# Kernel optimization log

Hardware: AMD Instinct MI355X
Metric: run time of the kernel (lower is better)

Reference implementation:

```python
import jax, jax.numpy as jnp
import numpy as np


def _dct_basis(n: int) -> jnp.ndarray:
    # Unnormalized DCT-II basis matching torch_dct.dct(norm=None):
    # X[k] = 2 * sum_n x[n] * cos(pi*(2n+1)*k / (2N))
    k = np.arange(n)[:, None]
    m = np.arange(n)[None, :]
    D = 2.0 * np.cos(np.pi * (2.0 * m + 1.0) * k / (2.0 * n))
    return jnp.asarray(D, dtype=jnp.float32)


def setup_inputs() -> dict:
    key = jax.random.key(0)
    img = jax.random.normal(key, (32, 3, 512, 512), dtype=jnp.float32)
    return {"img": img}


def reference(img) -> jnp.ndarray:
    B, C, H, W = img.shape
    Dh = _dct_basis(H)  # [H, H]
    Dw = _dct_basis(W)  # [W, W]
    x = img.astype(jnp.float32)
    # 2D DCT-II: Dh @ x @ Dw^T, batched over (B, C); fused /1000 scale.
    tmp = jnp.einsum('kh,bchw->bckw', Dh, x)
    out = jnp.einsum('bckw,lw->bckl', tmp, Dw) / 1000.0
    return out
```

## Files before the change

kernel.cpp:

```cpp
#include <hip/hip_runtime.h>
#include <hip/hip_bf16.h>
#include <stdint.h>

#define NPIX 512
#define NBC  96
#define NWG8 (NBC * 4)
#define NWG13 (NBC * 8)

typedef __attribute__((ext_vector_type(8))) short bf16x8;
typedef __attribute__((ext_vector_type(4))) float f32x4;
typedef __attribute__((ext_vector_type(8))) unsigned short u16x8;

__device__ __forceinline__ unsigned short f2bf(float f) {
    __hip_bfloat16 h = __float2bfloat16(f);
    union { __hip_bfloat16 h; unsigned short u; } v;
    v.h = h;
    return v.u;
}

#define GLD16(g, l) __builtin_amdgcn_global_load_lds( \
    (const __attribute__((address_space(1))) void*)(const void*)(g), \
    (__attribute__((address_space(3))) void*)(void*)(l), 16, 0, 0)

#define SBAR() do { __builtin_amdgcn_sched_barrier(0); \
                    __builtin_amdgcn_s_barrier(); \
                    __builtin_amdgcn_sched_barrier(0); } while (0)
#define LGKM0() do { asm volatile("s_waitcnt lgkmcnt(0)" ::: "memory"); \
                     __builtin_amdgcn_sched_barrier(0); } while (0)
#define SB0() __builtin_amdgcn_sched_barrier(0)
#define VMW(n) do { asm volatile("s_waitcnt vmcnt(" #n ")" ::: "memory"); } while (0)

__global__ void k_basis(unsigned short* __restrict__ D) {
    int idx = blockIdx.x * 256 + threadIdx.x;
    int k = idx >> 9, n = idx & 511;
    int m = ((2 * n + 1) * k) & 2047;
    float ang = (float)m * 3.06796157577128218e-03f;
    D[idx] = f2bf(2.0f * cosf(ang));
}

__global__ __launch_bounds__(512, 4) void k_s1x(
        const unsigned short* __restrict__ D,
        const float* __restrict__ X,
        unsigned short* __restrict__ sT) {
    __shared__ __align__(16) char LDS[81920];

    const int bid = blockIdx.x;
    const int nb  = (bid & 7) * (NWG13 / 8) + (bid >> 3);
    const int bc = nb >> 3, mt = (nb >> 2) & 1, nt = nb & 3;
    const int mA0 = mt * 256, nB0 = nt * 128;
    const unsigned short* Aimg = D;
    const float* Bimg = X + (size_t)bc * NPIX * NPIX;

    const int tid  = threadIdx.x;
    const int lane = tid & 63;
    const int wid  = tid >> 6;
    const int wr = wid >> 2, wc = wid & 3;
    const int rm = lane & 15;
    const int kq = lane >> 4;

    f32x4 acc[8][2] = {};
    bf16x8 a[4], b[2];

    auto stageA = [&](int kt, int p2, int H) {
        int c = tid;
        int rp = c >> 2, g = c & 3;
        int gs = g ^ ((rp >> 1) & 3);
        int row = ((rp >> 6) << 7) + H * 64 + (rp & 63);
        GLD16(Aimg + (size_t)(mA0 + row) * NPIX + kt * 32 + gs * 8,
              LDS + p2 * 16384 + H * 8192 + c * 16);
    };
    auto stageB = [&](int kt, int s3, int H) {
        int c = tid;
        int rp = c >> 3, g = c & 7;
        int gs = g ^ (rp & 7);
        int row = ((rp >> 5) << 6) + H * 32 + (rp & 31);
        GLD16(Bimg + (size_t)(nB0 + row) * NPIX + kt * 32 + gs * 4,
              LDS + 32768 + s3 * 16384 + H * 8192 + c * 16);
    };
    auto readA = [&](int p2, int mh) {
        const char* base = LDS + p2 * 16384 + mh * 8192;
        #pragma unroll
        for (int f = 0; f < 4; ++f) {
            int rp = wr * 64 + f * 16 + rm;
            int slot = kq ^ ((rm >> 1) & 3);
            a[f] = *(const bf16x8*)(base + rp * 64 + slot * 16);
        }
    };
    auto readB = [&](int s3) {
        const char* base = LDS + 32768 + s3 * 16384 + (wc & 1) * 8192;
        #pragma unroll
        for (int jj = 0; jj < 2; ++jj) {
            int rp = (wc >> 1) * 32 + jj * 16 + rm;
            const char* rb = base + rp * 128;
            f32x4 v0 = *(const f32x4*)(rb + (((kq * 2 + 0) ^ (rm & 7)) * 16));
            f32x4 v1 = *(const f32x4*)(rb + (((kq * 2 + 1) ^ (rm & 7)) * 16));
            bf16x8 t;
            t[0] = (short)f2bf(v0[0]); t[1] = (short)f2bf(v0[1]);
            t[2] = (short)f2bf(v0[2]); t[3] = (short)f2bf(v0[3]);
            t[4] = (short)f2bf(v1[0]); t[5] = (short)f2bf(v1[1]);
            t[6] = (short)f2bf(v1[2]); t[7] = (short)f2bf(v1[3]);
            b[jj] = t;
        }
    };
    auto mma = [&](int mh) {
        __builtin_amdgcn_s_setprio(1);
        #pragma unroll
        for (int f = 0; f < 4; ++f)
            #pragma unroll
            for (int jj = 0; jj < 2; ++jj)
                acc[mh * 4 + f][jj] = __builtin_amdgcn_mfma_f32_16x16x32_bf16(
                    a[f], b[jj], acc[mh * 4 + f][jj], 0, 0, 0);
        __builtin_amdgcn_s_setprio(0);
    };

    stageB(0, 0, 0); SB0();
    stageB(0, 0, 1); SB0();
    stageA(0, 0, 0); SB0();
    stageA(0, 0, 1); SB0();
    stageB(1, 1, 0); SB0();
    stageB(1, 1, 1); SB0();

    for (int T = 0; T < 14; ++T) {
        const int p2 = T & 1, p2n = p2 ^ 1;
        const int s3 = T % 3, s3b = (T + 2) % 3;
        VMW(3); SBAR();
        readA(p2, 0); readB(s3);
        stageA(T + 1, p2n, 0); SB0();
        stageB(T + 2, s3b, 0); SB0();
        LGKM0(); mma(0);
        VMW(3); SBAR();
        readA(p2, 1);
        stageA(T + 1, p2n, 1); SB0();
        stageB(T + 2, s3b, 1); SB0();
        LGKM0(); mma(1);
    }
    {
        VMW(3); SBAR();
        readA(0, 0); readB(2);
        stageA(15, 1, 0); SB0();
        LGKM0(); mma(0);
        VMW(2); SBAR();
        readA(0, 1);
        stageA(15, 1, 1); SB0();
        LGKM0(); mma(1);
    }
    {
        VMW(1); SBAR();
        readA(1, 0); readB(0);
        LGKM0(); mma(0);
        VMW(0); SBAR();
        readA(1, 1);
        LGKM0(); mma(1);
    }

    unsigned short* Co = sT + (size_t)bc * NPIX * NPIX;
    #pragma unroll
    for (int mh = 0; mh < 2; ++mh)
        #pragma unroll
        for (int f = 0; f < 4; ++f) {
            int l_ = mA0 + wr * 128 + mh * 64 + f * 16 + kq * 4;
            #pragma unroll
            for (int jj = 0; jj < 2; ++jj) {
                int h_ = nB0 + wc * 32 + jj * 16 + rm;
                f32x4 v = acc[mh * 4 + f][jj];
                #pragma unroll
                for (int r = 0; r < 4; ++r)
                    Co[(size_t)(l_ + r) * NPIX + h_] = f2bf(v[r]);
            }
        }
}

__global__ __launch_bounds__(512) void k_s2g(
        const unsigned short* __restrict__ D,
        const unsigned short* __restrict__ sT,
        float* __restrict__ Cv) {
    __shared__ __align__(16) char LDS[131072];

    const int bid = blockIdx.x;
    const int nb  = (bid & 7) * (NWG8 / 8) + (bid >> 3);
    const int bc = nb >> 2, mt = (nb >> 1) & 1, nt = nb & 1;
    const int mA0 = mt * 256, nB0 = nt * 256;
    const unsigned short* Aimg = D;
    const unsigned short* Bimg = sT + (size_t)bc * NPIX * NPIX;

    const int tid  = threadIdx.x;
    const int lane = tid & 63;
    const int wid  = tid >> 6;
    const int wr = wid >> 2, wc = wid & 3;
    const int rm = lane & 15;
    const int kq = lane >> 4;

    f32x4 acc[8][4] = {};
    bf16x8 a[4][2], b0[2][2], b1[2][2];

    auto stageA = [&](int kt, int p, int H) {
        char* dst = LDS + p * 32768 + H * 16384;
        #pragma unroll
        for (int it = 0; it < 2; ++it) {
            int c = it * 512 + tid;
            int rp = c >> 3, g = c & 7;
            int gs = g ^ (rp & 7);
            int row = ((rp >> 6) << 7) + H * 64 + (rp & 63);
            GLD16(Aimg + (size_t)(mA0 + row) * NPIX + kt * 64 + gs * 8, dst + c * 16);
        }
    };
    auto stageB = [&](int kt, int p, int H) {
        char* dst = LDS + 65536 + p * 32768 + H * 16384;
        #pragma unroll
        for (int it = 0; it < 2; ++it) {
            int c = it * 512 + tid;
            int rp = c >> 3, g = c & 7;
            int gs = g ^ (rp & 7);
            int row = ((rp >> 5) << 6) + H * 32 + (rp & 31);
            GLD16(Bimg + (size_t)(nB0 + row) * NPIX + kt * 64 + gs * 8, dst + c * 16);
        }
    };
    auto readA = [&](int p, int mh) {
        const char* base = LDS + p * 32768 + mh * 16384;
        #pragma unroll
        for (int f = 0; f < 4; ++f) {
            int rp = wr * 64 + f * 16 + rm;
            #pragma unroll
            for (int ks = 0; ks < 2; ++ks) {
                int slot = (ks * 4 + kq) ^ (rm & 7);
                a[f][ks] = *(const bf16x8*)(base + rp * 128 + slot * 16);
            }
        }
    };
    auto readB = [&](int p, int nh, bf16x8 (&b)[2][2]) {
        const char* base = LDS + 65536 + p * 32768 + nh * 16384;
        #pragma unroll
        for (int jj = 0; jj < 2; ++jj) {
            int rp = wc * 32 + jj * 16 + rm;
            #pragma unroll
            for (int ks = 0; ks < 2; ++ks) {
                int slot = (ks * 4 + kq) ^ (rm & 7);
                b[jj][ks] = *(const bf16x8*)(base + rp * 128 + slot * 16);
            }
        }
    };
    auto mma = [&](int mh, int nh, bf16x8 (&b)[2][2]) {
        __builtin_amdgcn_s_setprio(1);
        #pragma unroll
        for (int f = 0; f < 4; ++f)
            #pragma unroll
            for (int jj = 0; jj < 2; ++jj)
                #pragma unroll
                for (int ks = 0; ks < 2; ++ks)
                    acc[mh * 4 + f][nh * 2 + jj] = __builtin_amdgcn_mfma_f32_16x16x32_bf16(
                        a[f][ks], b[jj][ks], acc[mh * 4 + f][nh * 2 + jj], 0, 0, 0);
        __builtin_amdgcn_s_setprio(0);
    };

    stageA(0, 0, 0); stageB(0, 0, 0); stageB(0, 0, 1); stageA(0, 0, 1);

    for (int T = 0; T < 7; ++T) {
        const int p = T & 1, pn = p ^ 1;
        asm volatile("s_waitcnt vmcnt(4)" ::: "memory"); SBAR();
        readA(p, 0); readB(p, 0, b0); stageA(T + 1, pn, 0);
        LGKM0(); mma(0, 0, b0);
        asm volatile("s_waitcnt vmcnt(4)" ::: "memory"); SBAR();
        readB(p, 1, b1); stageB(T + 1, pn, 0);
        LGKM0(); mma(0, 1, b1);
        asm volatile("s_waitcnt vmcnt(4)" ::: "memory"); SBAR();
        readA(p, 1); stageB(T + 1, pn, 1);
        LGKM0(); mma(1, 0, b0);
        SBAR();
        stageA(T + 1, pn, 1);
        mma(1, 1, b1);
    }
    {
        asm volatile("s_waitcnt vmcnt(4)" ::: "memory"); SBAR();
        readA(1, 0); readB(1, 0, b0); LGKM0(); mma(0, 0, b0);
        asm volatile("s_waitcnt vmcnt(2)" ::: "memory"); SBAR();
        readB(1, 1, b1); LGKM0(); mma(0, 1, b1);
        asm volatile("s_waitcnt vmcnt(0)" ::: "memory"); SBAR();
        readA(1, 1); LGKM0(); mma(1, 0, b0);
        SBAR();
        mma(1, 1, b1);
    }

    float* Co = Cv + (size_t)bc * NPIX * NPIX;
    #pragma unroll
    for (int mh = 0; mh < 2; ++mh)
        #pragma unroll
        for (int f = 0; f < 4; ++f) {
            int k_ = mA0 + wr * 128 + mh * 64 + f * 16 + kq * 4;
            #pragma unroll
            for (int nh = 0; nh < 2; ++nh)
                #pragma unroll
                for (int jj = 0; jj < 2; ++jj) {
                    int l_ = nB0 + wc * 64 + (nh * 2 + jj) * 16 + rm;
                    f32x4 v = acc[mh * 4 + f][nh * 2 + jj];
                    #pragma unroll
                    for (int r = 0; r < 4; ++r)
                        Co[(size_t)(k_ + r) * NPIX + l_] = v[r] * 1.0e-3f;
                }
        }
}

extern "C" void kernel_launch(void* const* d_in, const int* in_sizes, int n_in,
                              void* d_out, int out_size, void* d_ws, size_t ws_size,
                              hipStream_t stream) {
    const float* img = (const float*)d_in[0];
    float* out = (float*)d_out;

    unsigned short* D  = (unsigned short*)d_ws;
    unsigned short* sT = (unsigned short*)((char*)d_ws + 512 * 1024);

    k_basis<<<dim3(512 * 512 / 256), dim3(256), 0, stream>>>(D);

    k_s1x<<<dim3(NWG13), dim3(512), 0, stream>>>(D, img, sT);

    k_s2g<<<dim3(NWG8), dim3(512), 0, stream>>>(D, sT, out);
}
```

Measured before the change: 84.39 us.

## Restructure first GEMM pipeline to one barrier per K-tile with full-tile staging

Replaces the half-tile staged pipeline, which had two barriers and two vmcnt waits per K-step plus a hand-peeled epilogue, with a single barrier per K-tile. Each thread issues all of the next tile's A and B global-to-LDS loads up front, then does both MFMA halves. The row-to-wave mapping of A and B is also reorganised: waves now own interleaved 64-row blocks of the output. This halves synchronisation points and simplifies the loop, at the cost of coarser overlap and bigger load bursts per barrier.

```diff
diff --git a/kernel.cpp b/kernel.cpp
--- a/kernel.cpp
+++ b/kernel.cpp
@@ -61,39 +61,44 @@
     f32x4 acc[8][2] = {};
     bf16x8 a[4], b[2];
 
-    auto stageA = [&](int kt, int p2, int H) {
-        int c = tid;
-        int rp = c >> 2, g = c & 3;
-        int gs = g ^ ((rp >> 1) & 3);
-        int row = ((rp >> 6) << 7) + H * 64 + (rp & 63);
-        GLD16(Aimg + (size_t)(mA0 + row) * NPIX + kt * 32 + gs * 8,
-              LDS + p2 * 16384 + H * 8192 + c * 16);
-    };
-    auto stageB = [&](int kt, int s3, int H) {
-        int c = tid;
-        int rp = c >> 3, g = c & 7;
-        int gs = g ^ (rp & 7);
-        int row = ((rp >> 5) << 6) + H * 32 + (rp & 31);
-        GLD16(Bimg + (size_t)(nB0 + row) * NPIX + kt * 32 + gs * 4,
-              LDS + 32768 + s3 * 16384 + H * 8192 + c * 16);
+    auto stageA = [&](int kt, int p2) {
+        #pragma unroll
+        for (int it = 0; it < 2; ++it) {
+            int c = it * 512 + tid;
+            int rp = c >> 2, g = c & 3;
+            int gs = g ^ ((rp >> 1) & 3);
+            int row = ((rp >> 7) << 7) + ((rp >> 6) & 1) * 64 + (rp & 63);
+            GLD16(Aimg + (size_t)(mA0 + row) * NPIX + kt * 32 + gs * 8,
+                  LDS + p2 * 16384 + c * 16);
+        }
+    };
+    auto stageB = [&](int kt, int s3) {
+        #pragma unroll
+        for (int it = 0; it < 2; ++it) {
+            int c = it * 512 + tid;
+            int rp = c >> 3, g = c & 7;
+            int gs = g ^ (rp & 7);
+            GLD16(Bimg + (size_t)(nB0 + rp) * NPIX + kt * 32 + gs * 4,
+                  LDS + 32768 + s3 * 16384 + c * 16);
+        }
     };
     auto readA = [&](int p2, int mh) {
         const char* base = LDS + p2 * 16384 + mh * 8192;
         #pragma unroll
         for (int f = 0; f < 4; ++f) {
-            int rp = wr * 64 + f * 16 + rm;
-            int slot = kq ^ ((rm >> 1) & 3);
-            a[f] = *(const bf16x8*)(base + rp * 64 + slot * 16);
-        }
+            int rp = mh * 128 + wr * 64 + f * 16 + rm;
+            int slot = kq ^ ((rp >> 1) & 3);
+            a[f] = *(const bf16x8*)(LDS + p2 * 16384 + rp * 64 + slot * 16);
+        }
+        (void)base;
     };
     auto readB = [&](int s3) {
-        const char* base = LDS + 32768 + s3 * 16384 + (wc & 1) * 8192;
         #pragma unroll
         for (int jj = 0; jj < 2; ++jj) {
-            int rp = (wc >> 1) * 32 + jj * 16 + rm;
-            const char* rb = base + rp * 128;
-            f32x4 v0 = *(const f32x4*)(rb + (((kq * 2 + 0) ^ (rm & 7)) * 16));
-            f32x4 v1 = *(const f32x4*)(rb + (((kq * 2 + 1) ^ (rm & 7)) * 16));
+            int rp = wc * 32 + jj * 16 + rm;
+            const char* rb = LDS + 32768 + s3 * 16384 + rp * 128;
+            f32x4 v0 = *(const f32x4*)(rb + (((kq * 2 + 0) ^ (rp & 7)) * 16));
+            f32x4 v1 = *(const f32x4*)(rb + (((kq * 2 + 1) ^ (rp & 7)) * 16));
             bf16x8 t;
             t[0] = (short)f2bf(v0[0]); t[1] = (short)f2bf(v0[1]);
             t[2] = (short)f2bf(v0[2]); t[3] = (short)f2bf(v0[3]);
@@ -113,43 +118,21 @@
         __builtin_amdgcn_s_setprio(0);
     };
 
-    stageB(0, 0, 0); SB0();
-    stageB(0, 0, 1); SB0();
-    stageA(0, 0, 0); SB0();
-    stageA(0, 0, 1); SB0();
-    stageB(1, 1, 0); SB0();
-    stageB(1, 1, 1); SB0();
-
-    for (int T = 0; T < 14; ++T) {
+    stageB(0, 0); SB0();
+    stageA(0, 0); SB0();
+    stageB(1, 1); SB0();
+
+    for (int T = 0; T < 16; ++T) {
         const int p2 = T & 1, p2n = p2 ^ 1;
         const int s3 = T % 3, s3b = (T + 2) % 3;
-        VMW(3); SBAR();
-        readA(p2, 0); readB(s3);
-        stageA(T + 1, p2n, 0); SB0();
-        stageB(T + 2, s3b, 0); SB0();
+        if (T < 15) { VMW(2); } else { VMW(0); }
+        SBAR();
+        if (T + 1 < 16) { stageA(T + 1, p2n); SB0(); }
+        if (T + 2 < 16) { stageB(T + 2, s3b); SB0(); }
+        readB(s3);
+        readA(p2, 0);
         LGKM0(); mma(0);
-        VMW(3); SBAR();
         readA(p2, 1);
-        stageA(T + 1, p2n, 1); SB0();
-        stageB(T + 2, s3b, 1); SB0();
-        LGKM0(); mma(1);
-    }
-    {
-        VMW(3); SBAR();
-        readA(0, 0); readB(2);
-        stageA(15, 1, 0); SB0();
-        LGKM0(); mma(0);
-        VMW(2); SBAR();
-        readA(0, 1);
-        stageA(15, 1, 1); SB0();
-        LGKM0(); mma(1);
-    }
-    {
-        VMW(1); SBAR();
-        readA(1, 0); readB(0);
-        LGKM0(); mma(0);
-        VMW(0); SBAR();
-        readA(1, 1);
         LGKM0(); mma(1);
     }
 
@@ -158,7 +141,7 @@
     for (int mh = 0; mh < 2; ++mh)
         #pragma unroll
         for (int f = 0; f < 4; ++f) {
-            int l_ = mA0 + wr * 128 + mh * 64 + f * 16 + kq * 4;
+            int l_ = mA0 + mh * 128 + wr * 64 + f * 16 + kq * 4;
             #pragma unroll
             for (int jj = 0; jj < 2; ++jj) {
                 int h_ = nB0 + wc * 32 + jj * 16 + rm;
```

Measured after the change: 84.10 us. About the same (-0.3%).
